# Kernel optimization log

Measured on AMD Instinct MI355X. Metric: run time of the kernel, lower is better.

The kernel has to match this reference:

```python
import jax, jax.numpy as jnp
import numpy as np

C = jnp.complex64

def _ry_mat(t):
    c = jnp.cos(t / 2).astype(C)
    s = jnp.sin(t / 2).astype(C)
    return jnp.stack([jnp.stack([c, -s], -1), jnp.stack([s, c], -1)], -2)

def _rx_mat(t):
    c = jnp.cos(t / 2).astype(C)
    s = (-1j) * jnp.sin(t / 2).astype(C)
    return jnp.stack([jnp.stack([c, s], -1), jnp.stack([s, c], -1)], -2)

def _rz_mat(t):
    em = jnp.exp(-1j * (t / 2).astype(C))
    ep = jnp.exp(1j * (t / 2).astype(C))
    z = jnp.zeros_like(em)
    return jnp.stack([jnp.stack([em, z], -1), jnp.stack([z, ep], -1)], -2)

def _apply_1q(psi, gate, w):
    # psi: [bsz, 2^n]; gate: [2,2] (shared) or [bsz,2,2] (per-sample)
    bsz = psi.shape[0]
    s = psi.reshape(bsz, 1 << w, 2, -1)  # wire w isolated on axis 2
    if gate.ndim == 2:
        out = jnp.einsum('ij,bljr->blir', gate, s)
    else:
        out = jnp.einsum('bij,bljr->blir', gate, s)
    return out.reshape(bsz, -1)

def _apply_cnot(psi, c, t):
    bsz = psi.shape[0]
    a, b = min(c, t), max(c, t)
    s = psi.reshape(bsz, 1 << a, 2, 1 << (b - a - 1), 2, -1)
    if c < t:
        # control on axis 2, target on axis 4; after slicing ctrl=1, target -> axis 3
        s = s.at[:, :, 1].set(jnp.flip(s[:, :, 1], axis=3))
    else:
        # control on axis 4, target on axis 2
        s = s.at[:, :, :, :, 1].set(jnp.flip(s[:, :, :, :, 1], axis=2))
    return s.reshape(bsz, -1)

def setup_inputs() -> dict:
    key = jax.random.key(0)
    k1, k2 = jax.random.split(key)
    bsz, n_wires, n_qlayers = 1024, 14, 4
    x_raw = jax.random.normal(k1, (bsz, n_wires), dtype=jnp.float32)
    angles = jax.random.normal(k2, (n_qlayers, n_wires, 3), dtype=jnp.float32) * 0.1
    return {"x_raw": x_raw, "angles": angles}

def reference(x_raw, angles):
    L, n, _ = angles.shape
    bsz = x_raw.shape[0]
    x_enc = jnp.tanh(x_raw[:, :n]) * jnp.pi  # [bsz, n]
    # |0...0> statevector, wire 0 is the most significant bit
    psi = jnp.zeros((bsz, 1 << n), dtype=C).at[:, 0].set(1.0)
    # RY encoding (per-sample angles)
    for w in range(n):
        psi = _apply_1q(psi, _ry_mat(x_enc[:, w]), w)
    # variational layers
    for k in range(L):
        for w in range(n):
            psi = _apply_1q(psi, _rx_mat(angles[k, w, 0]), w)
            psi = _apply_1q(psi, _ry_mat(angles[k, w, 1]), w)
            psi = _apply_1q(psi, _rz_mat(angles[k, w, 2]), w)
        for i in range(n - 1):
            psi = _apply_cnot(psi, i, i + 1)
        psi = _apply_cnot(psi, n - 1, 0)
    # <Z_0>: +|amp|^2 when bit0=0, -|amp|^2 when bit0=1
    p = jnp.abs(psi.reshape(bsz, 2, -1)) ** 2
    return (p[:, 0].sum(-1) - p[:, 1].sum(-1)).astype(jnp.float32)
```

## Files before the change

### kernel.cpp

```cpp
#include <hip/hip_runtime.h>
#include <cmath>
#include <cstdint>

#define NW       14
#define NST      (1 << NW)
#define THREADS  512
#define PRETHR   768
#define NPASS    12
#define WTP      512

typedef _Float16 f16;
typedef _Float16 f16x8 __attribute__((ext_vector_type(8)));
typedef float    f32x4 __attribute__((ext_vector_type(4)));
typedef unsigned short u16;

struct PassArg { u16 Mm[4]; u16 Mt[3]; u16 Mw[3]; };
struct Plan { PassArg ps[NPASS]; u16 initM[14]; u16 measR; u16 _pad; };

__device__ __forceinline__ float2 cmulf(float2 a, float2 b) {
    return make_float2(a.x * b.x - a.y * b.y, a.x * b.y + a.y * b.x);
}
__device__ __host__ __forceinline__ unsigned wtofs(unsigned m, unsigned q01) {
    return (m * 16 + q01 * 8) ^ (((m >> 2) & 1u) << 3);
}

__global__ __launch_bounds__(PRETHR)
void vqc_pre(const float* __restrict__ angles, f16* __restrict__ wt_g,
             float2* __restrict__ u0_g)
{
    __shared__ float2 G[4 * NW * 4];
    const int tid = threadIdx.x;

    if (tid < 4 * NW) {
        const int k = tid / NW, w = tid % NW;
        const float a  = angles[(k * NW + w) * 3 + 0];
        const float bb = angles[(k * NW + w) * 3 + 1];
        const float c  = angles[(k * NW + w) * 3 + 2];
        float sa, ca, sb, cb, sc, cc;
        sincosf(a * 0.5f, &sa, &ca);
        sincosf(bb * 0.5f, &sb, &cb);
        sincosf(c * 0.5f, &sc, &cc);
        float2 m00 = make_float2(cb * ca,  sb * sa);
        float2 m01 = make_float2(-sb * ca, -cb * sa);
        float2 m10 = make_float2(sb * ca,  -cb * sa);
        float2 m11 = make_float2(cb * ca,  -sb * sa);
        const float2 e0 = make_float2(cc, -sc), e1 = make_float2(cc, sc);
        const float2 u00 = cmulf(e0, m00), u01 = cmulf(e0, m01);
        const float2 u10 = cmulf(e1, m10), u11 = cmulf(e1, m11);
        const int gi = (k * NW + w) * 4;
        G[gi + 0] = u00; G[gi + 1] = u01; G[gi + 2] = u10; G[gi + 3] = u11;
        if (k == 0) {
            u0_g[w * 4 + 0] = u00; u0_g[w * 4 + 1] = u01;
            u0_g[w * 4 + 2] = u10; u0_g[w * 4 + 3] = u11;
        }
    }
    __syncthreads();

    {
        const int p = tid >> 6, l6 = tid & 63;
        const int ap = l6 & 15, ahalf = (l6 >> 4) & 1, dup = l6 >> 5;
        const int layer = (p >> 2) + 1, g = p & 3;

        float2 p3;
        if (g == 3) {
            p3 = make_float2((((ap >> 3) & 1) == ahalf) ? 1.f : 0.f, 0.f);
        } else {
            const int wire = 13 - (10 - 4 * g + 3);
            p3 = G[(layer * NW + wire) * 4 + ((ap >> 3) & 1) * 2 + ahalf];
        }
        float2 e0a, e0b, e1a, e1b, e2a, e2b;
        {
            const int r0 = ap & 1, r1 = (ap >> 1) & 1, r2 = (ap >> 2) & 1;
            if (g == 3) {
                const float2* G13 = G + (layer * NW + 13) * 4;
                const float2* G12 = G + (layer * NW + 12) * 4;
                e0a = G13[r0 * 2 + 0]; e0b = G13[r0 * 2 + 1];
                e1a = G12[r1 * 2 + 0]; e1b = G12[r1 * 2 + 1];
                e2a = make_float2(r2 == 0 ? 1.f : 0.f, 0.f);
                e2b = make_float2(r2 == 1 ? 1.f : 0.f, 0.f);
            } else {
                const float2* G0 = G + (layer * NW + (13 - (10 - 4 * g + 0))) * 4;
                const float2* G1 = G + (layer * NW + (13 - (10 - 4 * g + 1))) * 4;
                const float2* G2 = G + (layer * NW + (13 - (10 - 4 * g + 2))) * 4;
                e0a = G0[r0 * 2 + 0]; e0b = G0[r0 * 2 + 1];
                e1a = G1[r1 * 2 + 0]; e1b = G1[r1 * 2 + 1];
                e2a = G2[r2 * 2 + 0]; e2b = G2[r2 * 2 + 1];
            }
        }
        f16x8 frag;
        #pragma unroll
        for (int j2 = 0; j2 < 8; ++j2) {
            float2 v = cmulf(p3, (j2 & 4) ? e2b : e2a);
            v = cmulf(v, (j2 & 2) ? e1b : e1a);
            v = cmulf(v, (j2 & 1) ? e0b : e0a);
            frag[j2] = (f16)(dup ? v.y : v.x);
        }
        *(f16x8*)(wt_g + p * WTP + dup * 256 + wtofs(ap, ahalf)) = frag;
    }
}

__global__ __launch_bounds__(THREADS, 4)
void vqc_kernel(const float* __restrict__ x_raw, const f16* __restrict__ wt_g,
                const float2* __restrict__ u0_g, float* __restrict__ out, Plan pl)
{
    extern __shared__ char smem[];
    f16*    Sh  = (f16*)smem;
    f16*    Wt  = Sh + 2 * NST;
    float2* G0c = (float2*)(Wt + NPASS * WTP);
    float*  red = (float*)(G0c + 2 * NW);

    const int b   = blockIdx.x;
    const int tid = threadIdx.x;
    const int lane = tid & 63, wv = tid >> 6;
    const int q = lane >> 4, m = lane & 15;

    {
        const uint4* src = (const uint4*)wt_g;
        uint4* dst = (uint4*)Wt;
        dst[tid] = src[tid];
        if (tid < 256) dst[512 + tid] = src[512 + tid];
    }
    if (tid < NW) {
        const float xe = tanhf(x_raw[b * NW + tid]) * 3.14159265358979f;
        float se, ce;
        sincosf(xe * 0.5f, &se, &ce);
        const float2 u00 = u0_g[tid * 4 + 0], u01 = u0_g[tid * 4 + 1];
        const float2 u10 = u0_g[tid * 4 + 2], u11 = u0_g[tid * 4 + 3];
        G0c[tid * 2 + 0] = make_float2(u00.x * ce + u01.x * se, u00.y * ce + u01.y * se);
        G0c[tid * 2 + 1] = make_float2(u10.x * ce + u11.x * se, u10.y * ce + u11.y * se);
    }
    __syncthreads();

    {
        float2 common = make_float2(1.f, 0.f);
        #pragma unroll
        for (int bit = 0; bit < 9; ++bit) {
            const int w = 13 - bit;
            const float2 f = ((tid >> bit) & 1) ? G0c[w * 2 + 1] : G0c[w * 2 + 0];
            common = cmulf(common, f);
        }
        unsigned p9 = 0;
        #pragma unroll
        for (int bit = 0; bit < 9; ++bit)
            p9 ^= ((tid >> bit) & 1) ? (unsigned)pl.initM[bit] : 0u;
        float2 f0[2], f1[2], f2[2], f3[2], f4[2];
        f0[0] = G0c[4*2+0]; f0[1] = G0c[4*2+1];
        f1[0] = G0c[3*2+0]; f1[1] = G0c[3*2+1];
        f2[0] = G0c[2*2+0]; f2[1] = G0c[2*2+1];
        f3[0] = G0c[1*2+0]; f3[1] = G0c[1*2+1];
        f4[0] = G0c[0*2+0]; f4[1] = G0c[0*2+1];
        #pragma unroll
        for (int j = 0; j < 32; ++j) {
            float2 o = cmulf(cmulf(f0[j & 1], f1[(j >> 1) & 1]),
                             cmulf(f2[(j >> 2) & 1], f3[(j >> 3) & 1]));
            o = cmulf(o, f4[(j >> 4) & 1]);
            const float2 amp = cmulf(common, o);
            const unsigned ph = p9
                ^ ((j & 1) ? pl.initM[9]  : 0) ^ ((j & 2)  ? pl.initM[10] : 0)
                ^ ((j & 4) ? pl.initM[11] : 0) ^ ((j & 8)  ? pl.initM[12] : 0)
                ^ ((j & 16) ? pl.initM[13] : 0);
            Sh[ph]       = (f16)amp.x;
            Sh[ph + NST] = (f16)amp.y;
        }
    }
    __syncthreads();

    const unsigned plane_off = (unsigned)(q >> 1) << 14;
    const unsigned q01 = (unsigned)(q & 1);
    const f32x4 z4 = {0.f, 0.f, 0.f, 0.f};
    #pragma unroll
    for (int p = 0; p < NPASS; ++p) {
        const PassArg& P = pl.ps[p];
        const unsigned pm = ((m & 1) ? P.Mm[0] : 0) ^ ((m & 2) ? P.Mm[1] : 0)
                          ^ ((m & 4) ? P.Mm[2] : 0) ^ ((m & 8) ? P.Mm[3] : 0);
        const unsigned wb = ((wv & 1) ? P.Mw[0] : 0) ^ ((wv & 2) ? P.Mw[1] : 0)
                          ^ ((wv & 4) ? P.Mw[2] : 0);
        const unsigned b0 = pm ^ wb;
        const f16x8 tr = *(const f16x8*)(Wt + p * WTP +       wtofs((unsigned)m, q01));
        const f16x8 ti = *(const f16x8*)(Wt + p * WTP + 256 + wtofs((unsigned)m, q01));
        const f16x8 bf1 = (q < 2) ? tr : -ti;
        const f16x8 bf2 = (q < 2) ? ti : tr;
        unsigned sw[8];
        f16x8 av[8];
        #pragma unroll
        for (int tt = 0; tt < 8; ++tt) {
            sw[tt] = b0 ^ ((tt & 1) ? P.Mt[0] : 0)
                        ^ ((tt & 2) ? P.Mt[1] : 0)
                        ^ ((tt & 4) ? P.Mt[2] : 0);
            av[tt] = *(const f16x8*)(Sh + plane_off + (sw[tt] ^ (q01 << 3)));
        }
        __syncthreads();
        #pragma unroll
        for (int tt = 0; tt < 8; ++tt) {
            const f32x4 d1 = __builtin_amdgcn_mfma_f32_16x16x32_f16(av[tt], bf1, z4, 0, 0, 0);
            const f32x4 d2 = __builtin_amdgcn_mfma_f32_16x16x32_f16(av[tt], bf2, z4, 0, 0, 0);
            union { f16 h[4]; uint2 u; } c1, c2;
            #pragma unroll
            for (int r = 0; r < 4; ++r) { c1.h[r] = (f16)d1[r]; c2.h[r] = (f16)d2[r]; }
            const unsigned wu = sw[tt] ^ ((unsigned)q << 2);
            *(uint2*)(Sh + wu)       = c1.u;
            *(uint2*)(Sh + NST + wu) = c2.u;
        }
        __syncthreads();
    }

    float acc = 0.f;
    {
        const unsigned base = (unsigned)tid * 32;
        const int pb = __popc(base & (unsigned)pl.measR) & 1;
        #pragma unroll
        for (int cch = 0; cch < 4; ++cch) {
            const unsigned co = (unsigned)cch * 8;
            const f16x8 rr = *(const f16x8*)(Sh + (base ^ co));
            const f16x8 ii = *(const f16x8*)(Sh + NST + (base ^ co));
            #pragma unroll
            for (int e = 0; e < 8; ++e) {
                const float re = (float)rr[e], im = (float)ii[e];
                const float pw = fmaf(re, re, im * im);
                const int sgn = pb ^ (__popc((co | (unsigned)e) & (unsigned)pl.measR) & 1);
                acc += sgn ? -pw : pw;
            }
        }
    }
    #pragma unroll
    for (int off = 32; off > 0; off >>= 1) acc += __shfl_down(acc, off);
    if ((tid & 63) == 0) red[wv] = acc;
    __syncthreads();
    if (tid == 0) {
        float s = 0.f;
        #pragma unroll
        for (int i = 0; i < THREADS / 64; ++i) s += red[i];
        out[b] = s;
    }
}

struct GFm { u16 col[14]; };

static unsigned ringp_host(unsigned x) {
    unsigned s = x;
    s ^= s >> 1; s ^= s >> 2; s ^= s >> 4; s ^= s >> 8;
    s &= 0x3FFFu;
    return (s ^ ((s & 1u) << 13)) & 0x3FFFu;
}
static u16 gf_apply(const GFm& m, u16 v) {
    u16 r = 0;
    for (int b = 0; b < 14; ++b) if ((v >> b) & 1) r ^= m.col[b];
    return r;
}
static GFm gf_compose(const GFm& A, const GFm& B) {
    GFm C;
    for (int b = 0; b < 14; ++b) C.col[b] = gf_apply(A, B.col[b]);
    return C;
}
static void rows_from(const GFm& A, u16 r[14]) {
    for (int i = 0; i < 14; ++i) {
        u16 mm = 0;
        for (int b = 0; b < 14; ++b) mm |= (u16)(((A.col[b] >> i) & 1) << b);
        r[i] = mm;
    }
}
static GFm from_rows(const u16 r[14]) {
    GFm A;
    for (int b = 0; b < 14; ++b) {
        u16 c = 0;
        for (int i = 0; i < 14; ++i) c |= (u16)(((r[i] >> b) & 1) << i);
        A.col[b] = c;
    }
    return A;
}
static GFm gf_inv(const GFm& A) {
    u16 M[14], I[14];
    rows_from(A, M);
    for (int i = 0; i < 14; ++i) I[i] = (u16)(1u << i);
    for (int c = 0; c < 14; ++c) {
        int p = c;
        while (p < 14 && !((M[p] >> c) & 1)) ++p;
        if (p == 14) continue;
        u16 t = M[c]; M[c] = M[p]; M[p] = t;
        t = I[c]; I[c] = I[p]; I[p] = t;
        for (int r2 = 0; r2 < 14; ++r2)
            if (r2 != c && ((M[r2] >> c) & 1)) { M[r2] ^= M[c]; I[r2] ^= I[c]; }
    }
    return from_rows(I);
}

static void build_plan(Plan& pl) {
    GFm ring, ringInv;
    for (int b = 0; b < 14; ++b) ring.col[b] = (u16)ringp_host(1u << b);
    ringInv = gf_inv(ring);

    GFm phi;
    for (int j = 0; j < 4; ++j) phi.col[10 + j] = (u16)(1u << j);
    for (int j = 0; j < 4; ++j) phi.col[6 + j]  = (u16)(1u << (4 + j));
    for (int j = 0; j < 4; ++j) phi.col[2 + j]  = (u16)(1u << (8 + j));
    phi.col[0] = (u16)(1u << 12);
    phi.col[1] = (u16)(1u << 13);

    for (int b = 0; b < 14; ++b) pl.initM[b] = gf_apply(phi, ring.col[b]);

    const int gb[4][4] = {{10,11,12,13},{6,7,8,9},{2,3,4,5},{0,1,6,7}};

    for (int p = 0; p < NPASS; ++p) {
        const int g = p & 3;
        u16 uv[4];
        if (g < 3) for (int j = 0; j < 4; ++j) uv[j] = (u16)(1u << gb[g + 1][j]);
        else       for (int j = 0; j < 4; ++j) uv[j] = ringInv.col[10 + j];
        for (int j = 0; j < 4; ++j) pl.ps[p].Mm[j] = gf_apply(phi, uv[j]);

        u16 span[14]; int ns = 0;
        u16 tv[6]; int nt = 0;
        auto tryAdd = [&](u16 v) -> bool {
            bool ch = true;
            while (ch) {
                ch = false;
                for (int i = 0; i < ns; ++i) {
                    const int tb = 31 - __builtin_clz((unsigned)span[i]);
                    if ((v >> tb) & 1) { v ^= span[i]; ch = true; }
                }
            }
            if (!v) return false;
            span[ns++] = v;
            return true;
        };
        for (int j = 0; j < 4; ++j) tryAdd((u16)(1u << gb[g][j]));
        for (int j = 0; j < 4; ++j) tryAdd(uv[j]);
        for (int b2 = 0; b2 < 14 && nt < 6; ++b2)
            if (tryAdd((u16)(1u << b2))) tv[nt++] = (u16)(1u << b2);
        for (int i = 0; i < 3; ++i) pl.ps[p].Mt[i] = gf_apply(phi, tv[i]);
        for (int i = 0; i < 3; ++i) pl.ps[p].Mw[i] = gf_apply(phi, tv[i + 3]);

        GFm Bm;
        for (int j = 0; j < 4; ++j) Bm.col[j]     = (u16)(1u << gb[g][j]);
        for (int j = 0; j < 4; ++j) Bm.col[4 + j] = uv[j];
        for (int i = 0; i < 6; ++i) Bm.col[8 + i] = tv[i];
        GFm Binv = gf_inv(Bm);
        u16 img[14];
        for (int j = 0; j < 4; ++j) img[j]     = pl.ps[p].Mm[j];
        for (int j = 0; j < 4; ++j) img[4 + j] = (u16)(1u << j);
        for (int i = 0; i < 6; ++i) img[8 + i] = gf_apply(phi, tv[i]);
        GFm nphi;
        for (int b2 = 0; b2 < 14; ++b2) {
            const u16 coef = gf_apply(Binv, (u16)(1u << b2));
            u16 v = 0;
            for (int j = 0; j < 14; ++j) if ((coef >> j) & 1) v ^= img[j];
            nphi.col[b2] = v;
        }
        if (g == 3) nphi = gf_compose(nphi, ringInv);
        phi = nphi;
    }

    GFm pinv = gf_inv(phi);
    u16 rows[14];
    rows_from(pinv, rows);
    pl.measR = rows[13];
    pl._pad = 0;
}

static u16 swz_h(u16 v) {
    return (u16)(v ^ ((((v >> 6) ^ (v >> 9) ^ (v >> 11)) & 7u) << 3));
}
static u16 swzT_h(u16 r) {
    u16 o = r;
    if ((r >> 3) & 1) o ^= (u16)((1u << 6) | (1u << 9)  | (1u << 11));
    if ((r >> 4) & 1) o ^= (u16)((1u << 7) | (1u << 10) | (1u << 12));
    if ((r >> 5) & 1) o ^= (u16)((1u << 8) | (1u << 11) | (1u << 13));
    return o;
}
static void fold_swzu(Plan& pl) {
    for (int p = 0; p < NPASS; ++p) {
        for (int j = 0; j < 4; ++j) pl.ps[p].Mm[j] = swz_h(pl.ps[p].Mm[j]);
        for (int j = 0; j < 3; ++j) pl.ps[p].Mt[j] = swz_h(pl.ps[p].Mt[j]);
        for (int j = 0; j < 3; ++j) pl.ps[p].Mw[j] = swz_h(pl.ps[p].Mw[j]);
    }
    for (int b = 0; b < 14; ++b) pl.initM[b] = swz_h(pl.initM[b]);
    pl.measR = swzT_h(pl.measR);
}

extern "C" void kernel_launch(void* const* d_in, const int* in_sizes, int n_in,
                              void* d_out, int out_size, void* d_ws, size_t ws_size,
                              hipStream_t stream) {
    const float* x_raw  = (const float*)d_in[0];
    const float* angles = (const float*)d_in[1];
    float* out = (float*)d_out;
    const int bsz = in_sizes[0] / NW;

    Plan pl;
    build_plan(pl);
    fold_swzu(pl);

    f16*    wt_g = (f16*)d_ws;
    float2* u0_g = (float2*)((char*)d_ws + (size_t)NPASS * WTP * sizeof(f16));

    vqc_pre<<<dim3(1), dim3(PRETHR), 0, stream>>>(angles, wt_g, u0_g);

    const size_t lds = (size_t)2 * NST * sizeof(f16)
                     + (size_t)NPASS * WTP * sizeof(f16)
                     + (size_t)(2 * NW) * sizeof(float2)
                     + (size_t)(THREADS / 64) * sizeof(float);
    (void)hipFuncSetAttribute((const void*)vqc_kernel,
                              hipFuncAttributeMaxDynamicSharedMemorySize, (int)lds);
    vqc_kernel<<<dim3(bsz), dim3(THREADS), lds, stream>>>(x_raw, wt_g, u0_g, out, pl);
}
```

Before: 111.9 us.

## Use per-boundary searched LDS swizzles to reduce bank conflicts across passes

```diff
diff --git a/kernel.cpp b/kernel.cpp
--- a/kernel.cpp
+++ b/kernel.cpp
@@ -14,7 +14,7 @@
 typedef float    f32x4 __attribute__((ext_vector_type(4)));
 typedef unsigned short u16;
 
-struct PassArg { u16 Mm[4]; u16 Mt[3]; u16 Mw[3]; };
+struct PassArg { u16 Mm[4]; u16 Mt[3]; u16 Mw[3]; u16 Nm[4]; u16 Nt[3]; u16 Nw[3]; };
 struct Plan { PassArg ps[NPASS]; u16 initM[14]; u16 measR; u16 _pad; };
 
 __device__ __forceinline__ float2 cmulf(float2 a, float2 b) {
@@ -171,23 +171,25 @@
     #pragma unroll
     for (int p = 0; p < NPASS; ++p) {
         const PassArg& P = pl.ps[p];
-        const unsigned pm = ((m & 1) ? P.Mm[0] : 0) ^ ((m & 2) ? P.Mm[1] : 0)
-                          ^ ((m & 4) ? P.Mm[2] : 0) ^ ((m & 8) ? P.Mm[3] : 0);
-        const unsigned wb = ((wv & 1) ? P.Mw[0] : 0) ^ ((wv & 2) ? P.Mw[1] : 0)
-                          ^ ((wv & 4) ? P.Mw[2] : 0);
-        const unsigned b0 = pm ^ wb;
+        const unsigned b0R = ((m & 1) ? P.Mm[0] : 0) ^ ((m & 2) ? P.Mm[1] : 0)
+                           ^ ((m & 4) ? P.Mm[2] : 0) ^ ((m & 8) ? P.Mm[3] : 0)
+                           ^ ((wv & 1) ? P.Mw[0] : 0) ^ ((wv & 2) ? P.Mw[1] : 0)
+                           ^ ((wv & 4) ? P.Mw[2] : 0);
+        const unsigned b0W = ((m & 1) ? P.Nm[0] : 0) ^ ((m & 2) ? P.Nm[1] : 0)
+                           ^ ((m & 4) ? P.Nm[2] : 0) ^ ((m & 8) ? P.Nm[3] : 0)
+                           ^ ((wv & 1) ? P.Nw[0] : 0) ^ ((wv & 2) ? P.Nw[1] : 0)
+                           ^ ((wv & 4) ? P.Nw[2] : 0);
         const f16x8 tr = *(const f16x8*)(Wt + p * WTP +       wtofs((unsigned)m, q01));
         const f16x8 ti = *(const f16x8*)(Wt + p * WTP + 256 + wtofs((unsigned)m, q01));
         const f16x8 bf1 = (q < 2) ? tr : -ti;
         const f16x8 bf2 = (q < 2) ? ti : tr;
-        unsigned sw[8];
         f16x8 av[8];
         #pragma unroll
         for (int tt = 0; tt < 8; ++tt) {
-            sw[tt] = b0 ^ ((tt & 1) ? P.Mt[0] : 0)
-                        ^ ((tt & 2) ? P.Mt[1] : 0)
-                        ^ ((tt & 4) ? P.Mt[2] : 0);
-            av[tt] = *(const f16x8*)(Sh + plane_off + (sw[tt] ^ (q01 << 3)));
+            const unsigned swR = b0R ^ ((tt & 1) ? P.Mt[0] : 0)
+                                     ^ ((tt & 2) ? P.Mt[1] : 0)
+                                     ^ ((tt & 4) ? P.Mt[2] : 0);
+            av[tt] = *(const f16x8*)(Sh + plane_off + (swR ^ (q01 << 3)));
         }
         __syncthreads();
         #pragma unroll
@@ -197,7 +199,9 @@
             union { f16 h[4]; uint2 u; } c1, c2;
             #pragma unroll
             for (int r = 0; r < 4; ++r) { c1.h[r] = (f16)d1[r]; c2.h[r] = (f16)d2[r]; }
-            const unsigned wu = sw[tt] ^ ((unsigned)q << 2);
+            const unsigned wu = (b0W ^ ((tt & 1) ? P.Nt[0] : 0)
+                                     ^ ((tt & 2) ? P.Nt[1] : 0)
+                                     ^ ((tt & 4) ? P.Nt[2] : 0)) ^ ((unsigned)q << 2);
             *(uint2*)(Sh + wu)       = c1.u;
             *(uint2*)(Sh + NST + wu) = c2.u;
         }
@@ -210,7 +214,7 @@
         const int pb = __popc(base & (unsigned)pl.measR) & 1;
         #pragma unroll
         for (int cch = 0; cch < 4; ++cch) {
-            const unsigned co = (unsigned)cch * 8;
+            const unsigned co = ((unsigned)cch ^ ((unsigned)(lane >> 1) & 3u)) * 8;
             const f16x8 rr = *(const f16x8*)(Sh + (base ^ co));
             const f16x8 ii = *(const f16x8*)(Sh + NST + (base ^ co));
             #pragma unroll
@@ -284,7 +288,7 @@
     return from_rows(I);
 }
 
-static void build_plan(Plan& pl) {
+static void build_plan(Plan& pl, u16 rawMm[NPASS][4], u16 rawMt[NPASS][3], u16 rawMw[NPASS][3]) {
     GFm ring, ringInv;
     for (int b = 0; b < 14; ++b) ring.col[b] = (u16)ringp_host(1u << b);
     ringInv = gf_inv(ring);
@@ -305,7 +309,7 @@
         u16 uv[4];
         if (g < 3) for (int j = 0; j < 4; ++j) uv[j] = (u16)(1u << gb[g + 1][j]);
         else       for (int j = 0; j < 4; ++j) uv[j] = ringInv.col[10 + j];
-        for (int j = 0; j < 4; ++j) pl.ps[p].Mm[j] = gf_apply(phi, uv[j]);
+        for (int j = 0; j < 4; ++j) rawMm[p][j] = gf_apply(phi, uv[j]);
 
         u16 span[14]; int ns = 0;
         u16 tv[6]; int nt = 0;
@@ -326,8 +330,8 @@
         for (int j = 0; j < 4; ++j) tryAdd(uv[j]);
         for (int b2 = 0; b2 < 14 && nt < 6; ++b2)
             if (tryAdd((u16)(1u << b2))) tv[nt++] = (u16)(1u << b2);
-        for (int i = 0; i < 3; ++i) pl.ps[p].Mt[i] = gf_apply(phi, tv[i]);
-        for (int i = 0; i < 3; ++i) pl.ps[p].Mw[i] = gf_apply(phi, tv[i + 3]);
+        for (int i = 0; i < 3; ++i) rawMt[p][i] = gf_apply(phi, tv[i]);
+        for (int i = 0; i < 3; ++i) rawMw[p][i] = gf_apply(phi, tv[i + 3]);
 
         GFm Bm;
         for (int j = 0; j < 4; ++j) Bm.col[j]     = (u16)(1u << gb[g][j]);
@@ -335,7 +339,7 @@
         for (int i = 0; i < 6; ++i) Bm.col[8 + i] = tv[i];
         GFm Binv = gf_inv(Bm);
         u16 img[14];
-        for (int j = 0; j < 4; ++j) img[j]     = pl.ps[p].Mm[j];
+        for (int j = 0; j < 4; ++j) img[j]     = rawMm[p][j];
         for (int j = 0; j < 4; ++j) img[4 + j] = (u16)(1u << j);
         for (int i = 0; i < 6; ++i) img[8 + i] = gf_apply(phi, tv[i]);
         GFm nphi;
@@ -356,24 +360,54 @@
     pl._pad = 0;
 }
 
-static u16 swz_h(u16 v) {
-    return (u16)(v ^ ((((v >> 6) ^ (v >> 9) ^ (v >> 11)) & 7u) << 3));
-}
-static u16 swzT_h(u16 r) {
+static inline int par16(unsigned v) { return __builtin_parity(v); }
+static u16 psi_ap(u16 v, unsigned A, unsigned B) {
+    return (u16)(v ^ (par16(v & A) << 4) ^ (par16(v & B) << 5));
+}
+static u16 psi_T(u16 r, unsigned A, unsigned B) {
     u16 o = r;
-    if ((r >> 3) & 1) o ^= (u16)((1u << 6) | (1u << 9)  | (1u << 11));
-    if ((r >> 4) & 1) o ^= (u16)((1u << 7) | (1u << 10) | (1u << 12));
-    if ((r >> 5) & 1) o ^= (u16)((1u << 8) | (1u << 11) | (1u << 13));
+    if ((r >> 4) & 1) o ^= (u16)A;
+    if ((r >> 5) & 1) o ^= (u16)B;
     return o;
 }
-static void fold_swzu(Plan& pl) {
+static bool rank2ok(const u16* v, unsigned A, unsigned B) {
+    int seen = 0;
+    for (int j = 0; j < 4; ++j) {
+        const int b4 = ((v[j] >> 4) & 1) ^ par16(v[j] & A);
+        const int b5 = ((v[j] >> 5) & 1) ^ par16(v[j] & B);
+        const int val = b4 | (b5 << 1);
+        if (val) seen |= 1 << val;
+    }
+    const int cnt = ((seen >> 1) & 1) + ((seen >> 2) & 1) + ((seen >> 3) & 1);
+    return cnt >= 2;
+}
+
+static void finalize_plan(Plan& pl, u16 rawMm[NPASS][4], u16 rawMt[NPASS][3],
+                          u16 rawMw[NPASS][3]) {
+    unsigned psiA[NPASS + 1], psiB[NPASS + 1];
+    for (int bd = 0; bd <= NPASS; ++bd) {
+        unsigned bestA = 0, bestB = 0;
+        bool found = false;
+        for (unsigned a = 0; a < 256 && !found; ++a) {
+            for (unsigned b = 0; b < 256; ++b) {
+                const unsigned A = a << 6, B = b << 6;
+                const bool okR = (bd == NPASS) || rank2ok(rawMm[bd], A, B);
+                const bool okW = (bd == 0)     || rank2ok(rawMm[bd - 1], A, B);
+                if (okR && okW) { bestA = A; bestB = B; found = true; break; }
+            }
+        }
+        psiA[bd] = bestA; psiB[bd] = bestB;
+    }
     for (int p = 0; p < NPASS; ++p) {
-        for (int j = 0; j < 4; ++j) pl.ps[p].Mm[j] = swz_h(pl.ps[p].Mm[j]);
-        for (int j = 0; j < 3; ++j) pl.ps[p].Mt[j] = swz_h(pl.ps[p].Mt[j]);
-        for (int j = 0; j < 3; ++j) pl.ps[p].Mw[j] = swz_h(pl.ps[p].Mw[j]);
-    }
-    for (int b = 0; b < 14; ++b) pl.initM[b] = swz_h(pl.initM[b]);
-    pl.measR = swzT_h(pl.measR);
+        for (int j = 0; j < 4; ++j) pl.ps[p].Mm[j] = psi_ap(rawMm[p][j], psiA[p], psiB[p]);
+        for (int j = 0; j < 3; ++j) pl.ps[p].Mt[j] = psi_ap(rawMt[p][j], psiA[p], psiB[p]);
+        for (int j = 0; j < 3; ++j) pl.ps[p].Mw[j] = psi_ap(rawMw[p][j], psiA[p], psiB[p]);
+        for (int j = 0; j < 4; ++j) pl.ps[p].Nm[j] = psi_ap(rawMm[p][j], psiA[p+1], psiB[p+1]);
+        for (int j = 0; j < 3; ++j) pl.ps[p].Nt[j] = psi_ap(rawMt[p][j], psiA[p+1], psiB[p+1]);
+        for (int j = 0; j < 3; ++j) pl.ps[p].Nw[j] = psi_ap(rawMw[p][j], psiA[p+1], psiB[p+1]);
+    }
+    for (int b = 0; b < 14; ++b) pl.initM[b] = psi_ap(pl.initM[b], psiA[0], psiB[0]);
+    pl.measR = psi_T(pl.measR, psiA[NPASS], psiB[NPASS]);
 }
 
 extern "C" void kernel_launch(void* const* d_in, const int* in_sizes, int n_in,
@@ -385,8 +419,9 @@
     const int bsz = in_sizes[0] / NW;
 
     Plan pl;
-    build_plan(pl);
-    fold_swzu(pl);
+    u16 rawMm[NPASS][4], rawMt[NPASS][3], rawMw[NPASS][3];
+    build_plan(pl, rawMm, rawMt, rawMw);
+    finalize_plan(pl, rawMm, rawMt, rawMw);
 
     f16*    wt_g = (f16*)d_ws;
     float2* u0_g = (float2*)((char*)d_ws + (size_t)NPASS * WTP * sizeof(f16));
```

New measurement: 145.7 us. 30.2% more time.
